# Optimization experiments

Measured on AMD Instinct MI355X. Metric: run time of the kernel, lower is better.

The kernel has to match this reference:

```python
import jax, jax.numpy as jnp
import numpy as np

N_NODES = 100000
N_EDGES = 1600000
D_IN, D_HID, D_OUT = 128, 128, 64


def setup_inputs() -> dict:
    key = jax.random.key(0)
    ks = jax.random.split(key, 10)
    scale = 0.05
    return {
        "x": jax.random.normal(ks[0], (N_NODES, D_IN), jnp.float32),
        "edge_index": jax.random.randint(ks[1], (2, N_EDGES), 0, N_NODES, dtype=jnp.int64),
        "edge_weight": jax.random.uniform(ks[2], (N_EDGES,), jnp.float32),
        "W1": jax.random.normal(ks[3], (D_IN, D_HID), jnp.float32) * scale,
        "b1": jnp.zeros((D_HID,), jnp.float32),
        "W2": jax.random.normal(ks[4], (D_HID, D_HID), jnp.float32) * scale,
        "b2": jnp.zeros((D_HID,), jnp.float32),
        "W3": jax.random.normal(ks[5], (D_HID, D_OUT), jnp.float32) * scale,
        "b3": jnp.zeros((D_OUT,), jnp.float32),
    }


def reference(x, edge_index, edge_weight, W1, b1, W2, b2, W3, b3):
    N = x.shape[0]
    # GCN normalization with self-loops (PyG gcn_norm, add_self_loops=True, fill=1)
    loop = jnp.arange(N)
    row = jnp.concatenate([edge_index[0], loop])  # source nodes
    col = jnp.concatenate([edge_index[1], loop])  # target nodes
    w = jnp.concatenate([edge_weight, jnp.ones((N,), x.dtype)])
    deg = jax.ops.segment_sum(w, col, num_segments=N)
    dinv = jnp.where(deg > 0, jax.lax.rsqrt(deg), 0.0)
    norm = dinv[row] * w * dinv[col]  # [E+N]

    def gcn_conv(h, W, b):
        h = h @ W                                   # dense linear transform
        msg = h[row] * norm[:, None]                # gather + normalize
        return jax.ops.segment_sum(msg, col, num_segments=N) + b  # scatter-add

    h = jax.nn.relu(gcn_conv(x, W1, b1))   # dropout = identity (eval mode)
    h = jax.nn.relu(gcn_conv(h, W2, b2))
    return gcn_conv(h, W3, b3)
```

## Files before the change

kernel.cpp:

```cpp
#include <hip/hip_runtime.h>
#include <hip/hip_bf16.h>


static inline size_t align_up(size_t x, size_t a) { return (x + a - 1) & ~(a - 1); }

typedef _Float16 half8 __attribute__((ext_vector_type(8)));
typedef float f32x4 __attribute__((ext_vector_type(4)));

#define BSTRIDE 64

__device__ inline float2 h2_unpack(unsigned u) {
    union { unsigned u; _Float16 h[2]; } c; c.u = u;
    return make_float2((float)c.h[0], (float)c.h[1]);
}
__device__ inline unsigned h2_pack(float a, float b) {
    union { unsigned u; _Float16 h[2]; } c;
    c.h[0] = (_Float16)a; c.h[1] = (_Float16)b;
    return c.u;
}
__device__ inline float ent_w(unsigned v) {
    union { unsigned short s; _Float16 h; } c;
    c.s = (unsigned short)(v & 0x7FFFu);
    return (float)c.h;
}


__global__ void k_setup(unsigned long long* __restrict__ packed, int N,
                        const float* __restrict__ W1, _Float16* __restrict__ Wt1,
                        const float* __restrict__ W2, _Float16* __restrict__ Wt2,
                        const float* __restrict__ W3, _Float16* __restrict__ Wt3) {
    int i = blockIdx.x * blockDim.x + threadIdx.x;
    if (i < N) packed[i] = 0ull;
    if (i < 128 * 128) {
        int k = i >> 7, n = i & 127;
        Wt1[(size_t)n * 128 + k] = (_Float16)W1[i];
        Wt2[(size_t)n * 128 + k] = (_Float16)W2[i];
    }
    if (i < 128 * 64) {
        int k = i / 64, n = i % 64;
        Wt3[(size_t)n * 128 + k] = (_Float16)W3[i];
    }
}

__global__ void k_rank_scatter(const int* __restrict__ row, const int* __restrict__ col,
                               const float* __restrict__ w,
                               unsigned long long* __restrict__ packed,
                               unsigned* __restrict__ ent, int E) {
    int e = blockIdx.x * blockDim.x + threadIdx.x;
    if (e < E) {
        int c = col[e];
        float wf = w[e];
        unsigned long long add =
            (1ull << 40) | (unsigned long long)(wf * 16777216.0f);
        unsigned long long old = atomicAdd(&packed[c], add);
        unsigned rank = (unsigned)(old >> 40);
        if (rank < BSTRIDE) {
            union { _Float16 h; unsigned short s; } cv; cv.h = (_Float16)wf;
            ent[(size_t)c * BSTRIDE + rank] =
                ((unsigned)row[e] << 15) | (cv.s & 0x7FFFu);
        }
    }
}

__global__ void k_dinv(const unsigned long long* __restrict__ packed,
                       float* __restrict__ dinv, int N) {
    int i = blockIdx.x * blockDim.x + threadIdx.x;
    if (i < N) {
        unsigned long long p = packed[i];
        float deg = 1.0f + (float)(p & ((1ull << 40) - 1)) * (1.0f / 16777216.0f);
        dinv[i] = rsqrtf(deg);
    }
}


template <int NF, bool A_FP32>
__global__ __launch_bounds__(256) void k_gemm_mfma(
    const void* __restrict__ Aptr, const _Float16* __restrict__ Wt,
    const float* __restrict__ dinv, _Float16* __restrict__ G, int M) {
    const int K = 128;
    const int N = NF * 16;
    const int lane = threadIdx.x & 63;
    const int wv = threadIdx.x >> 6;
    const int mbase = blockIdx.x * 64 + wv * 16;
    const int r = lane & 15;
    const int g = lane >> 4;
    const int mrow = mbase + r;
    const int mc = (mrow < M) ? mrow : (M - 1);

    half8 a[4];
    if (A_FP32) {
        const float* A = (const float*)Aptr;
#pragma unroll
        for (int ks = 0; ks < 4; ++ks) {
            const float* p = A + (size_t)mc * K + ks * 32 + g * 8;
            float4 lo = *reinterpret_cast<const float4*>(p);
            float4 hi = *reinterpret_cast<const float4*>(p + 4);
            half8 h;
            h[0] = (_Float16)lo.x; h[1] = (_Float16)lo.y;
            h[2] = (_Float16)lo.z; h[3] = (_Float16)lo.w;
            h[4] = (_Float16)hi.x; h[5] = (_Float16)hi.y;
            h[6] = (_Float16)hi.z; h[7] = (_Float16)hi.w;
            a[ks] = h;
        }
    } else {
        const _Float16* A = (const _Float16*)Aptr;
#pragma unroll
        for (int ks = 0; ks < 4; ++ks)
            a[ks] = *reinterpret_cast<const half8*>(A + (size_t)mc * K + ks * 32 + g * 8);
    }

    f32x4 acc[NF];
#pragma unroll
    for (int nf = 0; nf < NF; ++nf) acc[nf] = (f32x4){0.f, 0.f, 0.f, 0.f};

#pragma unroll
    for (int nf = 0; nf < NF; ++nf) {
        const _Float16* wp = Wt + (size_t)(nf * 16 + r) * K + g * 8;
#pragma unroll
        for (int ks = 0; ks < 4; ++ks) {
            half8 b = *reinterpret_cast<const half8*>(wp + ks * 32);
            acc[nf] = __builtin_amdgcn_mfma_f32_16x16x32_f16(a[ks], b, acc[nf], 0, 0, 0);
        }
    }

#pragma unroll
    for (int reg = 0; reg < 4; ++reg) {
        int row = mbase + g * 4 + reg;
        if (row < M) {
            float di = dinv[row];
#pragma unroll
            for (int nf = 0; nf < NF; ++nf)
                G[(size_t)row * N + nf * 16 + r] = (_Float16)(acc[nf][reg] * di);
        }
    }
}


template <bool RELU>
__global__ __launch_bounds__(256) void k_agg128(
    const _Float16* __restrict__ G, const unsigned long long* __restrict__ packed,
    const unsigned* __restrict__ ent, const float* __restrict__ dinv,
    const float* __restrict__ bias, unsigned* __restrict__ Hout, int M) {
    const int lane = threadIdx.x & 63;
    const int half = lane >> 5;
    const int ln = lane & 31;
    const int wid = blockIdx.x * (blockDim.x >> 6) + (threadIdx.x >> 6);
    const int nw = gridDim.x * (blockDim.x >> 6);
    const uint2* G2 = reinterpret_cast<const uint2*>(G);
    const float4 bv = reinterpret_cast<const float4*>(bias)[ln];

    for (int i = wid; i < M; i += nw) {
        unsigned long long p = packed[i];
        int cnt = (int)(p >> 40); cnt = (cnt > BSTRIDE) ? BSTRIDE : cnt;
        float di = dinv[i];
        const unsigned* eb = ent + (size_t)i * BSTRIDE;
        uint2 sv = G2[(size_t)i * 32 + ln];
        float2 slo = h2_unpack(sv.x), shi = h2_unpack(sv.y);
        float a0[4], a1[4];
        a0[0] = half ? 0.f : slo.x; a0[1] = half ? 0.f : slo.y;
        a0[2] = half ? 0.f : shi.x; a0[3] = half ? 0.f : shi.y;
        a1[0] = 0.f; a1[1] = 0.f; a1[2] = 0.f; a1[3] = 0.f;

        for (int j = 0; j < cnt; j += 16) {
            unsigned v[8]; float wgt[8]; uint2 gv[8];
#pragma unroll
            for (int pz = 0; pz < 8; ++pz) {
                int je = j + 2 * pz + half;
                int jc = (je < cnt) ? je : (cnt - 1);
                jc = (jc < 0) ? 0 : jc;
                v[pz] = eb[jc];
            }
#pragma unroll
            for (int pz = 0; pz < 8; ++pz) {
                int je = j + 2 * pz + half;
                wgt[pz] = (je < cnt) ? ent_w(v[pz]) : 0.f;
                gv[pz] = G2[(size_t)(v[pz] >> 15) * 32 + ln];
            }
#pragma unroll
            for (int pz = 0; pz < 8; ++pz) {
                float2 lo = h2_unpack(gv[pz].x), hi = h2_unpack(gv[pz].y);
                if ((pz & 1) == 0) {
                    a0[0] = fmaf(wgt[pz], lo.x, a0[0]);
                    a0[1] = fmaf(wgt[pz], lo.y, a0[1]);
                    a0[2] = fmaf(wgt[pz], hi.x, a0[2]);
                    a0[3] = fmaf(wgt[pz], hi.y, a0[3]);
                } else {
                    a1[0] = fmaf(wgt[pz], lo.x, a1[0]);
                    a1[1] = fmaf(wgt[pz], lo.y, a1[1]);
                    a1[2] = fmaf(wgt[pz], hi.x, a1[2]);
                    a1[3] = fmaf(wgt[pz], hi.y, a1[3]);
                }
            }
        }
        float o[4];
#pragma unroll
        for (int k2 = 0; k2 < 4; ++k2) {
            float s = a0[k2] + a1[k2];
            s += __shfl_xor(s, 32, 64);
            float ov = fmaf(di, s, ((const float*)&bv)[k2]);
            o[k2] = RELU ? fmaxf(ov, 0.f) : ov;
        }
        if (half == 0) {
            uint2 w2;
            w2.x = h2_pack(o[0], o[1]);
            w2.y = h2_pack(o[2], o[3]);
            reinterpret_cast<uint2*>(Hout)[(size_t)i * 32 + ln] = w2;
        }
    }
}


__global__ __launch_bounds__(256) void k_agg64(
    const _Float16* __restrict__ G, const unsigned long long* __restrict__ packed,
    const unsigned* __restrict__ ent, const float* __restrict__ dinv,
    const float* __restrict__ bias, float* __restrict__ Hout, int M) {
    const int lane = threadIdx.x & 63;
    const int grp = lane >> 4;
    const int ln = lane & 15;
    const int sub = grp >> 1;
    const int par = grp & 1;
    const int wid = blockIdx.x * (blockDim.x >> 6) + (threadIdx.x >> 6);
    const int nw = gridDim.x * (blockDim.x >> 6);
    const uint2* G2 = reinterpret_cast<const uint2*>(G);
    const float4 bv = reinterpret_cast<const float4*>(bias)[ln];

    for (int base = wid * 2; base < M; base += nw * 2) {
        int i = base + sub;
        bool valid = (i < M);
        if (!valid) i = M - 1;
        unsigned long long p = packed[i];
        int cnt = (int)(p >> 40); cnt = (cnt > BSTRIDE) ? BSTRIDE : cnt;
        float di = dinv[i];
        const unsigned* eb = ent + (size_t)i * BSTRIDE;
        uint2 sv = G2[(size_t)i * 16 + ln];
        float2 slo = h2_unpack(sv.x), shi = h2_unpack(sv.y);
        float a0[4], a1[4];
        a0[0] = par ? 0.f : slo.x; a0[1] = par ? 0.f : slo.y;
        a0[2] = par ? 0.f : shi.x; a0[3] = par ? 0.f : shi.y;
        a1[0] = 0.f; a1[1] = 0.f; a1[2] = 0.f; a1[3] = 0.f;

        int cmax = cnt;
        cmax = max(cmax, __shfl_xor(cmax, 32, 64));

        for (int j = 0; j < cmax; j += 16) {
            unsigned v[8]; float wgt[8]; uint2 gv[8];
#pragma unroll
            for (int pz = 0; pz < 8; ++pz) {
                int je = j + 2 * pz + par;
                int jc = (je < cnt) ? je : (cnt - 1);
                jc = (jc < 0) ? 0 : jc;
                v[pz] = eb[jc];
            }
#pragma unroll
            for (int pz = 0; pz < 8; ++pz) {
                int je = j + 2 * pz + par;
                wgt[pz] = (je < cnt) ? ent_w(v[pz]) : 0.f;
                gv[pz] = G2[(size_t)(v[pz] >> 15) * 16 + ln];
            }
#pragma unroll
            for (int pz = 0; pz < 8; ++pz) {
                float2 lo = h2_unpack(gv[pz].x), hi = h2_unpack(gv[pz].y);
                if ((pz & 1) == 0) {
                    a0[0] = fmaf(wgt[pz], lo.x, a0[0]);
                    a0[1] = fmaf(wgt[pz], lo.y, a0[1]);
                    a0[2] = fmaf(wgt[pz], hi.x, a0[2]);
                    a0[3] = fmaf(wgt[pz], hi.y, a0[3]);
                } else {
                    a1[0] = fmaf(wgt[pz], lo.x, a1[0]);
                    a1[1] = fmaf(wgt[pz], lo.y, a1[1]);
                    a1[2] = fmaf(wgt[pz], hi.x, a1[2]);
                    a1[3] = fmaf(wgt[pz], hi.y, a1[3]);
                }
            }
        }
        float4 o;
        float* op = (float*)&o;
#pragma unroll
        for (int k2 = 0; k2 < 4; ++k2) {
            float s = a0[k2] + a1[k2];
            s += __shfl_xor(s, 16, 64);
            op[k2] = fmaf(di, s, ((const float*)&bv)[k2]);
        }
        if (valid && par == 0) {
            *reinterpret_cast<float4*>(Hout + (size_t)i * 64 + ln * 4) = o;
        }
    }
}


extern "C" void kernel_launch(void* const* d_in, const int* in_sizes, int n_in,
                              void* d_out, int out_size, void* d_ws, size_t ws_size,
                              hipStream_t stream) {
    const float* x  = (const float*)d_in[0];
    const int*   ei = (const int*)d_in[1];
    const float* ew = (const float*)d_in[2];
    const float* W1 = (const float*)d_in[3];
    const float* b1 = (const float*)d_in[4];
    const float* W2 = (const float*)d_in[5];
    const float* b2 = (const float*)d_in[6];
    const float* W3 = (const float*)d_in[7];
    const float* b3 = (const float*)d_in[8];
    float* out = (float*)d_out;

    const int DIN = 128, DHID = 128, DOUT = 64;
    const int N = in_sizes[0] / DIN;
    const int E = in_sizes[2];
    const int* e_row = ei;
    const int* e_col = ei + E;

    char* ws = (char*)d_ws;
    size_t off = 0;
    unsigned long long* packed = (unsigned long long*)(ws + off); off = align_up(off + (size_t)N * 8, 256);
    float* dinv   = (float*)(ws + off);    off = align_up(off + (size_t)N * 4, 256);
    unsigned* ent = (unsigned*)(ws + off); off = align_up(off + (size_t)N * BSTRIDE * 4, 256);
    _Float16* gbuf = (_Float16*)(ws + off); off = align_up(off + (size_t)N * DHID * 2, 256);
    _Float16* hbuf = (_Float16*)(ws + off); off = align_up(off + (size_t)N * DHID * 2, 256);
    _Float16* Wt1 = (_Float16*)(ws + off); off = align_up(off + (size_t)128 * 128 * 2, 256);
    _Float16* Wt2 = (_Float16*)(ws + off); off = align_up(off + (size_t)128 * 128 * 2, 256);
    _Float16* Wt3 = (_Float16*)(ws + off); off = align_up(off + (size_t)128 * 64 * 2, 256);
    (void)ws_size;

    const int nbN = (N + 255) / 256;
    const int nbE = (E + 255) / 256;

    k_setup<<<nbN, 256, 0, stream>>>(packed, N, W1, Wt1, W2, Wt2, W3, Wt3);
    k_rank_scatter<<<nbE, 256, 0, stream>>>(e_row, e_col, ew, packed, ent, E);
    k_dinv<<<nbN, 256, 0, stream>>>(packed, dinv, N);

    const int gemm_blocks = (N + 63) / 64;
    const int agg_blocks = 4096;

    k_gemm_mfma<8, true><<<gemm_blocks, 256, 0, stream>>>(x, Wt1, dinv, gbuf, N);
    k_agg128<true><<<agg_blocks, 256, 0, stream>>>(gbuf, packed, ent, dinv, b1,
                                                   (unsigned*)hbuf, N);

    k_gemm_mfma<8, false><<<gemm_blocks, 256, 0, stream>>>(hbuf, Wt2, dinv, gbuf, N);
    k_agg128<true><<<agg_blocks, 256, 0, stream>>>(gbuf, packed, ent, dinv, b2,
                                                   (unsigned*)hbuf, N);

    k_gemm_mfma<4, false><<<gemm_blocks, 256, 0, stream>>>(hbuf, Wt3, dinv, gbuf, N);
    k_agg64<<<agg_blocks, 256, 0, stream>>>(gbuf, packed, ent, dinv, b3, out, N);

    (void)n_in; (void)out_size;
}
```

Baseline: 383.8 us.

## Fuse edge scatter with first GEMM and fold source normalization into edge weights

Edge ranking/scatter, the first-layer GEMM (with W1 staged transposed in shared memory) and the weight transposes now run in one launch, with a memset replacing the zeroing kernel. A new per-node pass premultiplies each stored edge weight by the source node's dinv, so the GEMMs no longer scale rows by dinv. The self-loop term is scaled in the aggregation instead. The aggregation kernels are reworked to load 16-byte feature chunks per lane with more edges in flight, and use extra cross-lane shuffle reductions. The costs are an extra random-access pass over the edge table and storing the dinv-scaled weights in fp16.

```diff
diff --git a/kernel.cpp b/kernel.cpp
--- a/kernel.cpp
+++ b/kernel.cpp
@@ -23,17 +23,107 @@
     c.s = (unsigned short)(v & 0x7FFFu);
     return (float)c.h;
 }
-
-
-__global__ void k_setup(unsigned long long* __restrict__ packed, int N,
-                        const float* __restrict__ W1, _Float16* __restrict__ Wt1,
-                        const float* __restrict__ W2, _Float16* __restrict__ Wt2,
-                        const float* __restrict__ W3, _Float16* __restrict__ Wt3) {
-    int i = blockIdx.x * blockDim.x + threadIdx.x;
-    if (i < N) packed[i] = 0ull;
+__device__ inline unsigned ent_make(unsigned row, float w) {
+    union { _Float16 h; unsigned short s; } c; c.h = (_Float16)w;
+    return (row << 15) | (c.s & 0x7FFFu);
+}
+__device__ inline float fix2deg(unsigned long long p) {
+    return 1.0f + (float)(p & ((1ull << 40) - 1)) * (1.0f / 16777216.0f);
+}
+
+
+__global__ __launch_bounds__(256) void k_fuse(
+    const int* __restrict__ e_row, const int* __restrict__ e_col,
+    const float* __restrict__ ew,
+    unsigned long long* __restrict__ packed, unsigned* __restrict__ ent, int E,
+    const float* __restrict__ x, const float* __restrict__ W1,
+    _Float16* __restrict__ gbuf, int M,
+    const float* __restrict__ W2, _Float16* __restrict__ Wt2,
+    const float* __restrict__ W3, _Float16* __restrict__ Wt3,
+    int SCB, int G1B) {
+    __shared__ _Float16 WtL[64][136];
+    const int tid = threadIdx.x;
+    int bid = blockIdx.x;
+
+    if (bid < SCB) {
+        int e = bid * 256 + tid;
+        if (e < E) {
+            int c = e_col[e];
+            float wf = ew[e];
+            unsigned long long add =
+                (1ull << 40) | (unsigned long long)(wf * 16777216.0f);
+            unsigned long long old = atomicAdd(&packed[c], add);
+            unsigned rank = (unsigned)(old >> 40);
+            if (rank < BSTRIDE)
+                ent[(size_t)c * BSTRIDE + rank] = ent_make((unsigned)e_row[e], wf);
+        }
+        return;
+    }
+    bid -= SCB;
+    if (bid < G1B) {
+        const int K = 128;
+        const int lane = tid & 63;
+        const int wv = tid >> 6;
+        const int mbase = bid * 64 + wv * 16;
+        const int r = lane & 15;
+        const int g = lane >> 4;
+        const int mrow = mbase + r;
+        const int mc = (mrow < M) ? mrow : (M - 1);
+
+        half8 a[4];
+#pragma unroll
+        for (int ks = 0; ks < 4; ++ks) {
+            const float* p = x + (size_t)mc * K + ks * 32 + g * 8;
+            float4 lo = *reinterpret_cast<const float4*>(p);
+            float4 hi = *reinterpret_cast<const float4*>(p + 4);
+            half8 h;
+            h[0] = (_Float16)lo.x; h[1] = (_Float16)lo.y;
+            h[2] = (_Float16)lo.z; h[3] = (_Float16)lo.w;
+            h[4] = (_Float16)hi.x; h[5] = (_Float16)hi.y;
+            h[6] = (_Float16)hi.z; h[7] = (_Float16)hi.w;
+            a[ks] = h;
+        }
+
+        f32x4 acc[8];
+#pragma unroll
+        for (int nf = 0; nf < 8; ++nf) acc[nf] = (f32x4){0.f, 0.f, 0.f, 0.f};
+
+#pragma unroll
+        for (int half = 0; half < 2; ++half) {
+            for (int idx = tid; idx < 8192; idx += 256) {
+                int k = idx >> 6, n = idx & 63;
+                WtL[n][k] = (_Float16)W1[(size_t)k * 128 + half * 64 + n];
+            }
+            __syncthreads();
+#pragma unroll
+            for (int nf2 = 0; nf2 < 4; ++nf2) {
+#pragma unroll
+                for (int ks = 0; ks < 4; ++ks) {
+                    half8 b = *reinterpret_cast<const half8*>(
+                        &WtL[nf2 * 16 + r][ks * 32 + g * 8]);
+                    acc[half * 4 + nf2] =
+                        __builtin_amdgcn_mfma_f32_16x16x32_f16(a[ks], b,
+                                                               acc[half * 4 + nf2],
+                                                               0, 0, 0);
+                }
+            }
+            __syncthreads();
+        }
+#pragma unroll
+        for (int reg = 0; reg < 4; ++reg) {
+            int row = mbase + g * 4 + reg;
+            if (row < M) {
+#pragma unroll
+                for (int nf = 0; nf < 8; ++nf)
+                    gbuf[(size_t)row * 128 + nf * 16 + r] = (_Float16)acc[nf][reg];
+            }
+        }
+        return;
+    }
+    bid -= G1B;
+    int i = bid * 256 + tid;
     if (i < 128 * 128) {
         int k = i >> 7, n = i & 127;
-        Wt1[(size_t)n * 128 + k] = (_Float16)W1[i];
         Wt2[(size_t)n * 128 + k] = (_Float16)W2[i];
     }
     if (i < 128 * 64) {
@@ -42,41 +132,30 @@
     }
 }
 
-__global__ void k_rank_scatter(const int* __restrict__ row, const int* __restrict__ col,
-                               const float* __restrict__ w,
-                               unsigned long long* __restrict__ packed,
-                               unsigned* __restrict__ ent, int E) {
-    int e = blockIdx.x * blockDim.x + threadIdx.x;
-    if (e < E) {
-        int c = col[e];
-        float wf = w[e];
-        unsigned long long add =
-            (1ull << 40) | (unsigned long long)(wf * 16777216.0f);
-        unsigned long long old = atomicAdd(&packed[c], add);
-        unsigned rank = (unsigned)(old >> 40);
-        if (rank < BSTRIDE) {
-            union { _Float16 h; unsigned short s; } cv; cv.h = (_Float16)wf;
-            ent[(size_t)c * BSTRIDE + rank] =
-                ((unsigned)row[e] << 15) | (cv.s & 0x7FFFu);
-        }
-    }
-}
-
-__global__ void k_dinv(const unsigned long long* __restrict__ packed,
-                       float* __restrict__ dinv, int N) {
-    int i = blockIdx.x * blockDim.x + threadIdx.x;
-    if (i < N) {
-        unsigned long long p = packed[i];
-        float deg = 1.0f + (float)(p & ((1ull << 40) - 1)) * (1.0f / 16777216.0f);
-        dinv[i] = rsqrtf(deg);
-    }
-}
-
-
-template <int NF, bool A_FP32>
+
+__global__ __launch_bounds__(256) void k_scale(
+    const unsigned long long* __restrict__ packed,
+    unsigned* __restrict__ ent, float* __restrict__ dinv, int M) {
+    const int lane = threadIdx.x & 63;
+    const int i = (blockIdx.x * blockDim.x + threadIdx.x) >> 6;
+    if (i >= M) return;
+    unsigned long long p = packed[i];
+    int cnt = (int)(p >> 40); cnt = (cnt > BSTRIDE) ? BSTRIDE : cnt;
+    float di = rsqrtf(fix2deg(p));
+    if (lane == 0) dinv[i] = di;
+    if (lane < cnt) {
+        unsigned v = ent[(size_t)i * BSTRIDE + lane];
+        unsigned row = v >> 15;
+        float dr = rsqrtf(fix2deg(packed[row]));
+        ent[(size_t)i * BSTRIDE + lane] = ent_make(row, ent_w(v) * dr);
+    }
+}
+
+
+template <int NF>
 __global__ __launch_bounds__(256) void k_gemm_mfma(
-    const void* __restrict__ Aptr, const _Float16* __restrict__ Wt,
-    const float* __restrict__ dinv, _Float16* __restrict__ G, int M) {
+    const _Float16* __restrict__ A, const _Float16* __restrict__ Wt,
+    _Float16* __restrict__ G, int M) {
     const int K = 128;
     const int N = NF * 16;
     const int lane = threadIdx.x & 63;
@@ -88,26 +167,9 @@
     const int mc = (mrow < M) ? mrow : (M - 1);
 
     half8 a[4];
-    if (A_FP32) {
-        const float* A = (const float*)Aptr;
-#pragma unroll
-        for (int ks = 0; ks < 4; ++ks) {
-            const float* p = A + (size_t)mc * K + ks * 32 + g * 8;
-            float4 lo = *reinterpret_cast<const float4*>(p);
-            float4 hi = *reinterpret_cast<const float4*>(p + 4);
-            half8 h;
-            h[0] = (_Float16)lo.x; h[1] = (_Float16)lo.y;
-            h[2] = (_Float16)lo.z; h[3] = (_Float16)lo.w;
-            h[4] = (_Float16)hi.x; h[5] = (_Float16)hi.y;
-            h[6] = (_Float16)hi.z; h[7] = (_Float16)hi.w;
-            a[ks] = h;
-        }
-    } else {
-        const _Float16* A = (const _Float16*)Aptr;
-#pragma unroll
-        for (int ks = 0; ks < 4; ++ks)
-            a[ks] = *reinterpret_cast<const half8*>(A + (size_t)mc * K + ks * 32 + g * 8);
-    }
+#pragma unroll
+    for (int ks = 0; ks < 4; ++ks)
+        a[ks] = *reinterpret_cast<const half8*>(A + (size_t)mc * K + ks * 32 + g * 8);
 
     f32x4 acc[NF];
 #pragma unroll
@@ -127,10 +189,9 @@
     for (int reg = 0; reg < 4; ++reg) {
         int row = mbase + g * 4 + reg;
         if (row < M) {
-            float di = dinv[row];
 #pragma unroll
             for (int nf = 0; nf < NF; ++nf)
-                G[(size_t)row * N + nf * 16 + r] = (_Float16)(acc[nf][reg] * di);
+                G[(size_t)row * N + nf * 16 + r] = (_Float16)acc[nf][reg];
         }
     }
 }
@@ -142,69 +203,80 @@
     const unsigned* __restrict__ ent, const float* __restrict__ dinv,
     const float* __restrict__ bias, unsigned* __restrict__ Hout, int M) {
     const int lane = threadIdx.x & 63;
-    const int half = lane >> 5;
-    const int ln = lane & 31;
+    const int par = lane >> 4;
+    const int ln = lane & 15;
     const int wid = blockIdx.x * (blockDim.x >> 6) + (threadIdx.x >> 6);
     const int nw = gridDim.x * (blockDim.x >> 6);
-    const uint2* G2 = reinterpret_cast<const uint2*>(G);
-    const float4 bv = reinterpret_cast<const float4*>(bias)[ln];
+    const uint4* G4 = reinterpret_cast<const uint4*>(G);
+    const float4 bv0 = reinterpret_cast<const float4*>(bias)[2 * ln];
+    const float4 bv1 = reinterpret_cast<const float4*>(bias)[2 * ln + 1];
 
     for (int i = wid; i < M; i += nw) {
         unsigned long long p = packed[i];
         int cnt = (int)(p >> 40); cnt = (cnt > BSTRIDE) ? BSTRIDE : cnt;
         float di = dinv[i];
         const unsigned* eb = ent + (size_t)i * BSTRIDE;
-        uint2 sv = G2[(size_t)i * 32 + ln];
-        float2 slo = h2_unpack(sv.x), shi = h2_unpack(sv.y);
-        float a0[4], a1[4];
-        a0[0] = half ? 0.f : slo.x; a0[1] = half ? 0.f : slo.y;
-        a0[2] = half ? 0.f : shi.x; a0[3] = half ? 0.f : shi.y;
-        a1[0] = 0.f; a1[1] = 0.f; a1[2] = 0.f; a1[3] = 0.f;
-
+        uint4 sv = G4[(size_t)i * 16 + ln];
+        float acc[8];
+        {
+            float2 s0 = h2_unpack(sv.x), s1 = h2_unpack(sv.y);
+            float2 s2 = h2_unpack(sv.z), s3 = h2_unpack(sv.w);
+            float w0 = (par == 0) ? di : 0.f;
+            acc[0] = w0 * s0.x; acc[1] = w0 * s0.y;
+            acc[2] = w0 * s1.x; acc[3] = w0 * s1.y;
+            acc[4] = w0 * s2.x; acc[5] = w0 * s2.y;
+            acc[6] = w0 * s3.x; acc[7] = w0 * s3.y;
+        }
         for (int j = 0; j < cnt; j += 16) {
-            unsigned v[8]; float wgt[8]; uint2 gv[8];
-#pragma unroll
-            for (int pz = 0; pz < 8; ++pz) {
-                int je = j + 2 * pz + half;
-                int jc = (je < cnt) ? je : (cnt - 1);
-                jc = (jc < 0) ? 0 : jc;
-                v[pz] = eb[jc];
+            const int l = cnt - 1;
+            int j0 = j + par, j1 = j + 4 + par, j2 = j + 8 + par, j3 = j + 12 + par;
+            unsigned v0 = eb[j0 < cnt ? j0 : l];
+            unsigned v1 = eb[j1 < cnt ? j1 : l];
+            unsigned v2 = eb[j2 < cnt ? j2 : l];
+            unsigned v3 = eb[j3 < cnt ? j3 : l];
+            float w0 = (j0 < cnt) ? ent_w(v0) : 0.f;
+            float w1 = (j1 < cnt) ? ent_w(v1) : 0.f;
+            float w2 = (j2 < cnt) ? ent_w(v2) : 0.f;
+            float w3 = (j3 < cnt) ? ent_w(v3) : 0.f;
+            uint4 g0 = G4[(size_t)(v0 >> 15) * 16 + ln];
+            uint4 g1 = G4[(size_t)(v1 >> 15) * 16 + ln];
+            uint4 g2 = G4[(size_t)(v2 >> 15) * 16 + ln];
+            uint4 g3 = G4[(size_t)(v3 >> 15) * 16 + ln];
+#define ACC128(W, GV)                                                          \
+            {                                                                  \
+                float2 t0 = h2_unpack((GV).x), t1 = h2_unpack((GV).y);         \
+                float2 t2 = h2_unpack((GV).z), t3 = h2_unpack((GV).w);         \
+                acc[0] = fmaf((W), t0.x, acc[0]);                              \
+                acc[1] = fmaf((W), t0.y, acc[1]);                              \
+                acc[2] = fmaf((W), t1.x, acc[2]);                              \
+                acc[3] = fmaf((W), t1.y, acc[3]);                              \
+                acc[4] = fmaf((W), t2.x, acc[4]);                              \
+                acc[5] = fmaf((W), t2.y, acc[5]);                              \
+                acc[6] = fmaf((W), t3.x, acc[6]);                              \
+                acc[7] = fmaf((W), t3.y, acc[7]);                              \
             }
-#pragma unroll
-            for (int pz = 0; pz < 8; ++pz) {
-                int je = j + 2 * pz + half;
-                wgt[pz] = (je < cnt) ? ent_w(v[pz]) : 0.f;
-                gv[pz] = G2[(size_t)(v[pz] >> 15) * 32 + ln];
-            }
-#pragma unroll
-            for (int pz = 0; pz < 8; ++pz) {
-                float2 lo = h2_unpack(gv[pz].x), hi = h2_unpack(gv[pz].y);
-                if ((pz & 1) == 0) {
-                    a0[0] = fmaf(wgt[pz], lo.x, a0[0]);
-                    a0[1] = fmaf(wgt[pz], lo.y, a0[1]);
-                    a0[2] = fmaf(wgt[pz], hi.x, a0[2]);
-                    a0[3] = fmaf(wgt[pz], hi.y, a0[3]);
-                } else {
-                    a1[0] = fmaf(wgt[pz], lo.x, a1[0]);
-                    a1[1] = fmaf(wgt[pz], lo.y, a1[1]);
-                    a1[2] = fmaf(wgt[pz], hi.x, a1[2]);
-                    a1[3] = fmaf(wgt[pz], hi.y, a1[3]);
-                }
-            }
-        }
-        float o[4];
-#pragma unroll
-        for (int k2 = 0; k2 < 4; ++k2) {
-            float s = a0[k2] + a1[k2];
+            ACC128(w0, g0) ACC128(w1, g1) ACC128(w2, g2) ACC128(w3, g3)
+#undef ACC128
+        }
+        float o[8];
+        const float* bp0 = (const float*)&bv0;
+        const float* bp1 = (const float*)&bv1;
+#pragma unroll
+        for (int c8 = 0; c8 < 8; ++c8) {
+            float s = acc[c8];
+            s += __shfl_xor(s, 16, 64);
             s += __shfl_xor(s, 32, 64);
-            float ov = fmaf(di, s, ((const float*)&bv)[k2]);
-            o[k2] = RELU ? fmaxf(ov, 0.f) : ov;
-        }
-        if (half == 0) {
-            uint2 w2;
-            w2.x = h2_pack(o[0], o[1]);
-            w2.y = h2_pack(o[2], o[3]);
-            reinterpret_cast<uint2*>(Hout)[(size_t)i * 32 + ln] = w2;
+            float b = (c8 < 4) ? bp0[c8] : bp1[c8 - 4];
+            float ov = fmaf(di, s, b);
+            o[c8] = RELU ? fmaxf(ov, 0.f) : ov;
+        }
+        if (par == 0) {
+            uint4 w4;
+            w4.x = h2_pack(o[0], o[1]);
+            w4.y = h2_pack(o[2], o[3]);
+            w4.z = h2_pack(o[4], o[5]);
+            w4.w = h2_pack(o[6], o[7]);
+            reinterpret_cast<uint4*>(Hout)[(size_t)i * 16 + ln] = w4;
         }
     }
 }
@@ -215,74 +287,71 @@
     const unsigned* __restrict__ ent, const float* __restrict__ dinv,
     const float* __restrict__ bias, float* __restrict__ Hout, int M) {
     const int lane = threadIdx.x & 63;
-    const int grp = lane >> 4;
-    const int ln = lane & 15;
-    const int sub = grp >> 1;
-    const int par = grp & 1;
+    const int par = lane >> 3;
+    const int ln = lane & 7;
     const int wid = blockIdx.x * (blockDim.x >> 6) + (threadIdx.x >> 6);
     const int nw = gridDim.x * (blockDim.x >> 6);
-    const uint2* G2 = reinterpret_cast<const uint2*>(G);
-    const float4 bv = reinterpret_cast<const float4*>(bias)[ln];
-
-    for (int base = wid * 2; base < M; base += nw * 2) {
-        int i = base + sub;
-        bool valid = (i < M);
-        if (!valid) i = M - 1;
+    const uint4* G4 = reinterpret_cast<const uint4*>(G);
+    const float4 bv0 = reinterpret_cast<const float4*>(bias)[2 * ln];
+    const float4 bv1 = reinterpret_cast<const float4*>(bias)[2 * ln + 1];
+
+    for (int i = wid; i < M; i += nw) {
         unsigned long long p = packed[i];
         int cnt = (int)(p >> 40); cnt = (cnt > BSTRIDE) ? BSTRIDE : cnt;
         float di = dinv[i];
         const unsigned* eb = ent + (size_t)i * BSTRIDE;
-        uint2 sv = G2[(size_t)i * 16 + ln];
-        float2 slo = h2_unpack(sv.x), shi = h2_unpack(sv.y);
-        float a0[4], a1[4];
-        a0[0] = par ? 0.f : slo.x; a0[1] = par ? 0.f : slo.y;
-        a0[2] = par ? 0.f : shi.x; a0[3] = par ? 0.f : shi.y;
-        a1[0] = 0.f; a1[1] = 0.f; a1[2] = 0.f; a1[3] = 0.f;
-
-        int cmax = cnt;
-        cmax = max(cmax, __shfl_xor(cmax, 32, 64));
-
-        for (int j = 0; j < cmax; j += 16) {
-            unsigned v[8]; float wgt[8]; uint2 gv[8];
-#pragma unroll
-            for (int pz = 0; pz < 8; ++pz) {
-                int je = j + 2 * pz + par;
-                int jc = (je < cnt) ? je : (cnt - 1);
-                jc = (jc < 0) ? 0 : jc;
-                v[pz] = eb[jc];
+        uint4 sv = G4[(size_t)i * 8 + ln];
+        float acc[8];
+        {
+            float2 s0 = h2_unpack(sv.x), s1 = h2_unpack(sv.y);
+            float2 s2 = h2_unpack(sv.z), s3 = h2_unpack(sv.w);
+            float w0 = (par == 0) ? di : 0.f;
+            acc[0] = w0 * s0.x; acc[1] = w0 * s0.y;
+            acc[2] = w0 * s1.x; acc[3] = w0 * s1.y;
+            acc[4] = w0 * s2.x; acc[5] = w0 * s2.y;
+            acc[6] = w0 * s3.x; acc[7] = w0 * s3.y;
+        }
+        for (int j = 0; j < cnt; j += 16) {
+            const int l = cnt - 1;
+            int j0 = j + par, j1 = j + 8 + par;
+            unsigned v0 = eb[j0 < cnt ? j0 : l];
+            unsigned v1 = eb[j1 < cnt ? j1 : l];
+            float w0 = (j0 < cnt) ? ent_w(v0) : 0.f;
+            float w1 = (j1 < cnt) ? ent_w(v1) : 0.f;
+            uint4 g0 = G4[(size_t)(v0 >> 15) * 8 + ln];
+            uint4 g1 = G4[(size_t)(v1 >> 15) * 8 + ln];
+#define ACC64(W, GV)                                                           \
+            {                                                                  \
+                float2 t0 = h2_unpack((GV).x), t1 = h2_unpack((GV).y);         \
+                float2 t2 = h2_unpack((GV).z), t3 = h2_unpack((GV).w);         \
+                acc[0] = fmaf((W), t0.x, acc[0]);                              \
+                acc[1] = fmaf((W), t0.y, acc[1]);                              \
+                acc[2] = fmaf((W), t1.x, acc[2]);                              \
+                acc[3] = fmaf((W), t1.y, acc[3]);                              \
+                acc[4] = fmaf((W), t2.x, acc[4]);                              \
+                acc[5] = fmaf((W), t2.y, acc[5]);                              \
+                acc[6] = fmaf((W), t3.x, acc[6]);                              \
+                acc[7] = fmaf((W), t3.y, acc[7]);                              \
             }
-#pragma unroll
-            for (int pz = 0; pz < 8; ++pz) {
-                int je = j + 2 * pz + par;
-                wgt[pz] = (je < cnt) ? ent_w(v[pz]) : 0.f;
-                gv[pz] = G2[(size_t)(v[pz] >> 15) * 16 + ln];
-            }
-#pragma unroll
-            for (int pz = 0; pz < 8; ++pz) {
-                float2 lo = h2_unpack(gv[pz].x), hi = h2_unpack(gv[pz].y);
-                if ((pz & 1) == 0) {
-                    a0[0] = fmaf(wgt[pz], lo.x, a0[0]);
-                    a0[1] = fmaf(wgt[pz], lo.y, a0[1]);
-                    a0[2] = fmaf(wgt[pz], hi.x, a0[2]);
-                    a0[3] = fmaf(wgt[pz], hi.y, a0[3]);
-                } else {
-                    a1[0] = fmaf(wgt[pz], lo.x, a1[0]);
-                    a1[1] = fmaf(wgt[pz], lo.y, a1[1]);
-                    a1[2] = fmaf(wgt[pz], hi.x, a1[2]);
-                    a1[3] = fmaf(wgt[pz], hi.y, a1[3]);
-                }
-            }
-        }
-        float4 o;
-        float* op = (float*)&o;
-#pragma unroll
-        for (int k2 = 0; k2 < 4; ++k2) {
-            float s = a0[k2] + a1[k2];
+            ACC64(w0, g0) ACC64(w1, g1)
+#undef ACC64
+        }
+        float o[8];
+        const float* bp0 = (const float*)&bv0;
+        const float* bp1 = (const float*)&bv1;
+#pragma unroll
+        for (int c8 = 0; c8 < 8; ++c8) {
+            float s = acc[c8];
+            s += __shfl_xor(s, 8, 64);
             s += __shfl_xor(s, 16, 64);
-            op[k2] = fmaf(di, s, ((const float*)&bv)[k2]);
-        }
-        if (valid && par == 0) {
-            *reinterpret_cast<float4*>(Hout + (size_t)i * 64 + ln * 4) = o;
+            s += __shfl_xor(s, 32, 64);
+            o[c8] = fmaf(di, s, (c8 < 4) ? bp0[c8] : bp1[c8 - 4]);
+        }
+        if (par == 0) {
+            float4 q0 = make_float4(o[0], o[1], o[2], o[3]);
+            float4 q1 = make_float4(o[4], o[5], o[6], o[7]);
+            *reinterpret_cast<float4*>(Hout + (size_t)i * 64 + ln * 8) = q0;
+            *reinterpret_cast<float4*>(Hout + (size_t)i * 64 + ln * 8 + 4) = q1;
         }
     }
 }
@@ -302,7 +371,7 @@
     const float* b3 = (const float*)d_in[8];
     float* out = (float*)d_out;
 
-    const int DIN = 128, DHID = 128, DOUT = 64;
+    const int DIN = 128, DHID = 128;
     const int N = in_sizes[0] / DIN;
     const int E = in_sizes[2];
     const int* e_row = ei;
@@ -315,30 +384,28 @@
     unsigned* ent = (unsigned*)(ws + off); off = align_up(off + (size_t)N * BSTRIDE * 4, 256);
     _Float16* gbuf = (_Float16*)(ws + off); off = align_up(off + (size_t)N * DHID * 2, 256);
     _Float16* hbuf = (_Float16*)(ws + off); off = align_up(off + (size_t)N * DHID * 2, 256);
-    _Float16* Wt1 = (_Float16*)(ws + off); off = align_up(off + (size_t)128 * 128 * 2, 256);
     _Float16* Wt2 = (_Float16*)(ws + off); off = align_up(off + (size_t)128 * 128 * 2, 256);
     _Float16* Wt3 = (_Float16*)(ws + off); off = align_up(off + (size_t)128 * 64 * 2, 256);
     (void)ws_size;
 
-    const int nbN = (N + 255) / 256;
-    const int nbE = (E + 255) / 256;
-
-    k_setup<<<nbN, 256, 0, stream>>>(packed, N, W1, Wt1, W2, Wt2, W3, Wt3);
-    k_rank_scatter<<<nbE, 256, 0, stream>>>(e_row, e_col, ew, packed, ent, E);
-    k_dinv<<<nbN, 256, 0, stream>>>(packed, dinv, N);
-
-    const int gemm_blocks = (N + 63) / 64;
+    const int SCB = (E + 255) / 256;
+    const int G1B = (N + 63) / 64;
     const int agg_blocks = 4096;
 
-    k_gemm_mfma<8, true><<<gemm_blocks, 256, 0, stream>>>(x, Wt1, dinv, gbuf, N);
+    hipMemsetAsync(packed, 0, (size_t)N * 8, stream);
+
+    k_fuse<<<SCB + G1B + 64, 256, 0, stream>>>(
+        e_row, e_col, ew, packed, ent, E,
+        x, W1, gbuf, N, W2, Wt2, W3, Wt3, SCB, G1B);
+
+    k_scale<<<(N * 64 + 255) / 256, 256, 0, stream>>>(packed, ent, dinv, N);
+
     k_agg128<true><<<agg_blocks, 256, 0, stream>>>(gbuf, packed, ent, dinv, b1,
                                                    (unsigned*)hbuf, N);
-
-    k_gemm_mfma<8, false><<<gemm_blocks, 256, 0, stream>>>(hbuf, Wt2, dinv, gbuf, N);
+    k_gemm_mfma<8><<<G1B, 256, 0, stream>>>(hbuf, Wt2, gbuf, N);
     k_agg128<true><<<agg_blocks, 256, 0, stream>>>(gbuf, packed, ent, dinv, b2,
                                                    (unsigned*)hbuf, N);
-
-    k_gemm_mfma<4, false><<<gemm_blocks, 256, 0, stream>>>(hbuf, Wt3, dinv, gbuf, N);
+    k_gemm_mfma<4><<<G1B, 256, 0, stream>>>(hbuf, Wt3, gbuf, N);
     k_agg64<<<agg_blocks, 256, 0, stream>>>(gbuf, packed, ent, dinv, b3, out, N);
 
     (void)n_in; (void)out_size;
```

Result: slower. 404.9 us (+5.5%).
